# Kernel optimization log

Measured on AMD Instinct MI355X. Metric: run time of the kernel, lower is better.

Reference implementation:

```python
import jax, jax.numpy as jnp
import numpy as np

B, K, L, D = 64, 49, 200, 36  # batch, ref time points, seq len, n variables
INIT_TIME, PRIOR_HOURS = 0.0, 48.0


def setup_inputs() -> dict:
    key = jax.random.key(0)
    ks = jax.random.split(key, 9)
    X = jax.random.normal(ks[0], (B, L, D), dtype=jnp.float32)
    T = jax.random.uniform(ks[1], (B, L, D), dtype=jnp.float32) * PRIOR_HOURS
    M = (jax.random.uniform(ks[2], (B, L, D)) > 0.5).astype(jnp.float32)
    PD = jax.random.uniform(ks[3], (B, L, D), dtype=jnp.float32)
    # learned params per ALNNLayer.build (glorot-like small init)
    def glorot(k, shape):
        fan = sum(shape)
        lim = jnp.sqrt(6.0 / fan)
        return jax.random.uniform(k, shape, jnp.float32, -lim, lim)
    alpha = glorot(ks[4], (K, 1, 1))
    w_v = glorot(ks[5], (K, L, D))
    w_t = glorot(ks[6], (K, L, D, 4))
    b_v = glorot(ks[7], (K, 1, D))
    b_t = glorot(ks[8], (K, L, D, 1))
    return {"X": X, "T": T, "M": M, "PD": PD,
            "alpha": alpha, "w_v": w_v, "w_t": w_t, "b_v": b_v, "b_t": b_t}


def reference(X, T, M, PD, alpha, w_v, w_t, b_v, b_t):
    k = alpha.shape[0]
    # reference time points [K,1,1]
    ref_time = jnp.linspace(INIT_TIME, PRIOR_HOURS, k, dtype=jnp.float32).reshape(k, 1, 1)
    # broadcast [B,1,L,D] against [K,1,1] -> [B,K,L,D]
    dist = jnp.abs(T[:, None, :, :] - ref_time)           # type_distance == 'abs'
    kernel = jnp.exp(-jax.nn.relu(alpha) * dist)          # [B,K,L,D]
    intensity = jax.nn.relu(X[:, None, :, :] * kernel)    # [B,K,L,D]
    shp = intensity.shape
    # 4-channel concat on a trailing axis: [B,K,L,D,4]
    c = jnp.stack([
        jnp.broadcast_to(X[:, None, :, :], shp),
        intensity,
        jnp.broadcast_to(M[:, None, :, :], shp),
        jnp.broadcast_to(PD[:, None, :, :], shp),
    ], axis=-1)
    # stage 1: reduce_sum(w_t*c + b_t, axis=4); b_t broadcast over 4 channels -> contributes 4*b_t
    s1 = jax.nn.relu(jnp.einsum('bklds,klds->bkld', c, w_t) + 4.0 * b_t[..., 0])
    # stage 2: reduce_sum(w_v*s1 + b_v, axis=2); b_v [K,1,D] broadcast over L -> contributes L*b_v
    n_l = s1.shape[2]
    out = jax.nn.relu(jnp.einsum('bkld,kld->bkd', s1, w_v) + jnp.float32(n_l) * b_v[:, 0, :])
    return out  # [B,K,D]
```

## Files before the change

### kernel.cpp

```cpp
#include <hip/hip_runtime.h>

#define NB 64
#define NK 49
#define NL 200
#define ND 36
#define LD (NL*ND)

#define AT_FLOATS  (LD*NB*4)
#define WPK_FLOATS (LD*NK*6)
#define WPK_OFF   AT_FLOATS
#define WS_PACK_BYTES ((size_t)(AT_FLOATS + WPK_FLOATS) * 4)

#define LOG2E 1.44269504088896f

#if __has_builtin(__builtin_amdgcn_exp2f)
#define EXP2F(x) __builtin_amdgcn_exp2f(x)
#else
#define EXP2F(x) __expf((x) * 0.6931471805599453f)
#endif

__global__ __launch_bounds__(256) void alnn_pack(
    const float* __restrict__ X, const float* __restrict__ T,
    const float* __restrict__ M, const float* __restrict__ PD,
    const float* __restrict__ w_v, const float4* __restrict__ w_t,
    const float* __restrict__ b_t, float* __restrict__ ws)
{
    __shared__ float tile[9440];
    const int bid = blockIdx.x, t = threadIdx.x;

    if (bid < 225) {
        const int ld0 = bid * 32;
        const int ld = t & 31, bq = t >> 5;
        const float* src[4] = {X, T, M, PD};
        #pragma unroll
        for (int a = 0; a < 4; a++) {
            const float* A = src[a];
            for (int b = bq; b < 64; b += 8)
                tile[(a * 64 + b) * 33 + ld] = A[(size_t)b * LD + ld0 + ld];
        }
        __syncthreads();
        float4* At4 = (float4*)ws;
        const int b = t & 63, ldq = t >> 6;
        #pragma unroll
        for (int r = 0; r < 8; r++) {
            const int l_local = ldq * 8 + r;
            const int ldg = ld0 + l_local;
            const int l = ldg / ND, d = ldg - l * ND;
            float4 v;
            v.x = tile[(0 * 64 + b) * 33 + l_local];
            v.y = tile[(1 * 64 + b) * 33 + l_local];
            v.z = tile[(2 * 64 + b) * 33 + l_local];
            v.w = tile[(3 * 64 + b) * 33 + l_local];
            At4[((size_t)d * NL + l) * 64 + b] = v;
        }
    } else {
        const int ld0 = (bid - 225) * 32;
        const int ld = t & 31, kq = t >> 5;
        for (int k = kq; k < NK; k += 8) {
            const float4 wt = w_t[(size_t)k * LD + ld0 + ld];
            const float  bt = b_t[(size_t)k * LD + ld0 + ld];
            const float  wv = w_v[(size_t)k * LD + ld0 + ld];
            float* w = tile + ld * 295 + k * 6;
            w[0] = wt.x; w[1] = wt.y; w[2] = wt.z; w[3] = wt.w;
            w[4] = 4.0f * bt; w[5] = wv;
        }
        __syncthreads();
        float* Wpk = ws + WPK_OFF;
        for (int i = t; i < 7 * 32 * 42; i += 256) {
            const int ks = i / 1344, rem = i - ks * 1344;
            const int l_local = rem / 42, c = rem - l_local * 42;
            const int ldg = ld0 + l_local;
            const int l = ldg / ND, d = ldg - l * ND;
            Wpk[(((size_t)d * 7 + ks) * NL + l) * 42 + c] =
                tile[l_local * 295 + ks * 42 + c];
        }
    }
}

__global__ __launch_bounds__(1024) void alnn_main5(
    const float* __restrict__ ws_ro, const float* __restrict__ alpha,
    const float* __restrict__ b_v, float* __restrict__ out)
{
    __shared__ float red[16 * 7 * 64];

    const int orig = blockIdx.x;
    const int xcd  = orig & 7, slot = orig >> 3;
    const int base = (xcd < 4) ? xcd * 32 : 128 + (xcd - 4) * 31;
    const int job  = base + slot;

    const int d  = job / 7, ks = job - (job / 7) * 7;
    const int t  = threadIdx.x;
    const int b  = t & 63;
    const int w  = __builtin_amdgcn_readfirstlane(t >> 6);
    const int k0 = ks * 7;

    const float4* At4 = (const float4*)ws_ro + (size_t)d * NL * 64;
    const float*  Ws  = ws_ro + WPK_OFF + ((size_t)d * 7 + ks) * NL * 42;

    float arn[7], rk[7];
    #pragma unroll
    for (int kk = 0; kk < 7; kk++) {
        arn[kk] = -fmaxf(alpha[k0 + kk], 0.0f) * LOG2E;
        rk[kk]  = (float)(k0 + kk);
    }

    float acc[7] = {0, 0, 0, 0, 0, 0, 0};

    const int len  = (w < 8) ? 13 : 12;
    const int lbeg = (w < 8) ? 13 * w : 104 + 12 * (w - 8);

    for (int ll = 0; ll < len; ll++) {
        const int l = lbeg + ll;
        const float4 av = At4[(size_t)l * 64 + b];
        const float xp = fmaxf(av.x, 0.0f);
        const float* wr = Ws + (size_t)l * 42;
        #pragma unroll
        for (int kk = 0; kk < 7; kk++) {
            const float dist = fabsf(av.y - rk[kk]);
            const float e    = EXP2F(arn[kk] * dist);
            float s = fmaf(wr[kk*6+0], av.x,
                      fmaf(wr[kk*6+1], xp * e,
                      fmaf(wr[kk*6+2], av.z,
                      fmaf(wr[kk*6+3], av.w, wr[kk*6+4]))));
            acc[kk] = fmaf(wr[kk*6+5], fmaxf(s, 0.0f), acc[kk]);
        }
    }

    #pragma unroll
    for (int kk = 0; kk < 7; kk++)
        red[(w * 7 + kk) * 64 + b] = acc[kk];
    __syncthreads();

    if (w < 7) {
        const int kk = w, k = k0 + kk;
        float sum = 0.0f;
        #pragma unroll
        for (int ww = 0; ww < 16; ww++)
            sum += red[(ww * 7 + kk) * 64 + b];
        out[((size_t)b * NK + k) * ND + d] =
            fmaxf(sum + 200.0f * b_v[k * ND + d], 0.0f);
    }
}

__global__ __launch_bounds__(256) void alnn_fused_kernel(
    const float* __restrict__ X, const float* __restrict__ T,
    const float* __restrict__ M, const float* __restrict__ PD,
    const float* __restrict__ alpha, const float* __restrict__ w_v,
    const float4* __restrict__ w_t, const float* __restrict__ b_v,
    const float* __restrict__ b_t, float* __restrict__ out)
{
    const int bk = blockIdx.x;
    const int k  = bk % NK;
    const int b  = bk / NK;
    const int t  = threadIdx.x;

    __shared__ float part[7][ND];

    const float alpha_k = fmaxf(alpha[k], 0.0f);
    const float refk    = (float)k;

    if (t < 7 * ND) {
        const int d = t % ND;
        const int j = t / ND;
        const float*  Xp  = X   + (size_t)b * LD + d;
        const float*  Tp  = T   + (size_t)b * LD + d;
        const float*  Mp  = M   + (size_t)b * LD + d;
        const float*  Pp  = PD  + (size_t)b * LD + d;
        const float*  wvp = w_v + (size_t)k * LD + d;
        const float*  btp = b_t + (size_t)k * LD + d;
        const float4* wtp = w_t + (size_t)k * LD + d;

        float acc = 0.0f;
        for (int l = j; l < NL; l += 7) {
            const int o = l * ND;
            const float x  = Xp[o];
            const float tt = Tp[o];
            const float m  = Mp[o];
            const float pd = Pp[o];
            const float4 wv4 = wtp[o];
            const float bt = btp[o];
            const float dist  = fabsf(tt - refk);
            const float e     = __expf(-alpha_k * dist);
            const float inten = fmaxf(x * e, 0.0f);
            float s = fmaf(wv4.x, x, fmaf(wv4.y, inten, fmaf(wv4.z, m, fmaf(wv4.w, pd, 4.0f * bt))));
            s = fmaxf(s, 0.0f);
            acc = fmaf(wvp[o], s, acc);
        }
        part[j][d] = acc;
    }
    __syncthreads();

    if (t < ND) {
        float sum = 0.0f;
        #pragma unroll
        for (int j = 0; j < 7; ++j) sum += part[j][t];
        sum += (float)NL * b_v[k * ND + t];
        out[(size_t)bk * ND + t] = fmaxf(sum, 0.0f);
    }
}

extern "C" void kernel_launch(void* const* d_in, const int* in_sizes, int n_in,
                              void* d_out, int out_size, void* d_ws, size_t ws_size,
                              hipStream_t stream) {
    const float* X     = (const float*)d_in[0];
    const float* T     = (const float*)d_in[1];
    const float* M     = (const float*)d_in[2];
    const float* PD    = (const float*)d_in[3];
    const float* alpha = (const float*)d_in[4];
    const float* w_v   = (const float*)d_in[5];
    const float* w_t   = (const float*)d_in[6];
    const float* b_v   = (const float*)d_in[7];
    const float* b_t   = (const float*)d_in[8];
    float* out = (float*)d_out;
    float* ws  = (float*)d_ws;

    if (ws_size >= WS_PACK_BYTES) {
        alnn_pack<<<450, 256, 0, stream>>>(X, T, M, PD, w_v, (const float4*)w_t, b_t, ws);
        alnn_main5<<<252, 1024, 0, stream>>>(ws, alpha, b_v, out);
    } else {
        alnn_fused_kernel<<<NB * NK, 256, 0, stream>>>(
            X, T, M, PD, alpha, w_v, (const float4*)w_t, b_v, b_t, out);
    }
}
```

Before: 28.00 us.

## Fuse pack and main kernels into one cooperative kernel with grid sync

Replaces the two-launch pack-then-compute pipeline with a single cooperative kernel. Each block gathers its own slice of w_t/b_t/w_v directly into LDS, so the packed weight buffer in global memory is no longer written and re-read. The first 225 blocks transpose the activations into the workspace, followed by a grid-wide sync and the same compute/reduce as before. It also adds unroll-by-2 on the l loop. In exchange it adds grid-sync overhead and a large LDS footprint per block, and it depends on the cooperative launch succeeding, with a fallback to the old path if it does not.

```diff
diff --git a/kernel.cpp b/kernel.cpp
--- a/kernel.cpp
+++ b/kernel.cpp
@@ -1,4 +1,7 @@
 #include <hip/hip_runtime.h>
+#include <hip/hip_cooperative_groups.h>
+
+namespace cg = cooperative_groups;
 
 #define NB 64
 #define NK 49
@@ -9,6 +12,7 @@
 #define AT_FLOATS  (LD*NB*4)
 #define WPK_FLOATS (LD*NK*6)
 #define WPK_OFF   AT_FLOATS
+#define WS_MIN_BYTES  ((size_t)AT_FLOATS * 4)
 #define WS_PACK_BYTES ((size_t)(AT_FLOATS + WPK_FLOATS) * 4)
 
 #define LOG2E 1.44269504088896f
@@ -18,6 +22,118 @@
 #else
 #define EXP2F(x) __expf((x) * 0.6931471805599453f)
 #endif
+
+__global__ __launch_bounds__(1024, 4) void alnn_coop2(
+    const float* __restrict__ X, const float* __restrict__ T,
+    const float* __restrict__ M, const float* __restrict__ PD,
+    const float* __restrict__ alpha, const float* __restrict__ w_v,
+    const float4* __restrict__ w_t4, const float* __restrict__ b_v,
+    const float* __restrict__ b_t, float* __restrict__ out,
+    float* __restrict__ ws)
+{
+    __shared__ float tile[4 * 64 * 33];
+    __shared__ float wl[NL * 44];
+    __shared__ float red[16 * 7 * 64];
+
+    const int orig = blockIdx.x, t = threadIdx.x;
+
+    const int xcd  = orig & 7, slot = orig >> 3;
+    const int base = (xcd < 4) ? xcd * 32 : 128 + (xcd - 4) * 31;
+    const int job  = base + slot;
+    const int d = job / 7, ks = job - (job / 7) * 7;
+    const int k0 = ks * 7;
+
+    for (int i = t; i < 1400; i += 1024) {
+        const int kk = i / NL, l = i - kk * NL;
+        const size_t src = (size_t)(k0 + kk) * LD + l * ND + d;
+        const float4 wt = w_t4[src];
+        const float  bt = b_t[src];
+        const float  wv = w_v[src];
+        float* wp = wl + l * 44 + kk * 6;
+        wp[0] = wt.x; wp[1] = wt.y; wp[2] = wt.z; wp[3] = wt.w;
+        wp[4] = 4.0f * bt; wp[5] = wv;
+    }
+
+    if (orig < 225) {
+        const int ld0 = orig * 32;
+        const int ld = t & 31, bq = t >> 5;
+        const float* srcs[4] = {X, T, M, PD};
+        #pragma unroll
+        for (int a = 0; a < 4; a++) {
+            const float* A = srcs[a];
+            #pragma unroll
+            for (int b = bq; b < 64; b += 32)
+                tile[(a * 64 + b) * 33 + ld] = A[(size_t)b * LD + ld0 + ld];
+        }
+        __syncthreads();
+        float4* At4w = (float4*)ws;
+        const int b = t & 63, ldq = t >> 6;
+        #pragma unroll
+        for (int r = 0; r < 2; r++) {
+            const int ll = ldq * 2 + r;
+            const int ldg = ld0 + ll;
+            const int l = ldg / ND, dd = ldg - l * ND;
+            float4 v;
+            v.x = tile[(0 * 64 + b) * 33 + ll];
+            v.y = tile[(1 * 64 + b) * 33 + ll];
+            v.z = tile[(2 * 64 + b) * 33 + ll];
+            v.w = tile[(3 * 64 + b) * 33 + ll];
+            At4w[((size_t)dd * NL + l) * 64 + b] = v;
+        }
+    }
+
+    cg::this_grid().sync();
+
+    const int b = t & 63;
+    const int w = __builtin_amdgcn_readfirstlane(t >> 6);
+
+    const float4* At4 = (const float4*)ws + (size_t)d * NL * 64;
+
+    float arn[7], rk[7];
+    #pragma unroll
+    for (int kk = 0; kk < 7; kk++) {
+        arn[kk] = -fmaxf(alpha[k0 + kk], 0.0f) * LOG2E;
+        rk[kk]  = (float)(k0 + kk);
+    }
+
+    float acc[7] = {0, 0, 0, 0, 0, 0, 0};
+
+    const int len  = (w < 8) ? 13 : 12;
+    const int lbeg = (w < 8) ? 13 * w : 104 + 12 * (w - 8);
+
+    #pragma unroll 2
+    for (int ll = 0; ll < len; ll++) {
+        const int l = lbeg + ll;
+        const float4 av = At4[(size_t)l * 64 + b];
+        const float xp = fmaxf(av.x, 0.0f);
+        const float* wr = wl + l * 44;
+        #pragma unroll
+        for (int kk = 0; kk < 7; kk++) {
+            const float dist = fabsf(av.y - rk[kk]);
+            const float e    = EXP2F(arn[kk] * dist);
+            float s = fmaf(wr[kk*6+0], av.x,
+                      fmaf(wr[kk*6+1], xp * e,
+                      fmaf(wr[kk*6+2], av.z,
+                      fmaf(wr[kk*6+3], av.w, wr[kk*6+4]))));
+            acc[kk] = fmaf(wr[kk*6+5], fmaxf(s, 0.0f), acc[kk]);
+        }
+    }
+
+    #pragma unroll
+    for (int kk = 0; kk < 7; kk++)
+        red[(w * 7 + kk) * 64 + b] = acc[kk];
+    __syncthreads();
+
+    if (w < 7) {
+        const int kk = w, k = k0 + kk;
+        float sum = 0.0f;
+        #pragma unroll
+        for (int ww = 0; ww < 16; ww++)
+            sum += red[(ww * 7 + kk) * 64 + b];
+        out[((size_t)b * NK + k) * ND + d] =
+            fmaxf(sum + 200.0f * b_v[k * ND + d], 0.0f);
+    }
+}
 
 __global__ __launch_bounds__(256) void alnn_pack(
     const float* __restrict__ X, const float* __restrict__ T,
@@ -109,6 +225,7 @@
     const int len  = (w < 8) ? 13 : 12;
     const int lbeg = (w < 8) ? 13 * w : 104 + 12 * (w - 8);
 
+    #pragma unroll 2
     for (int ll = 0; ll < len; ll++) {
         const int l = lbeg + ll;
         const float4 av = At4[(size_t)l * 64 + b];
@@ -214,6 +331,16 @@
     float* out = (float*)d_out;
     float* ws  = (float*)d_ws;
 
+    if (ws_size >= WS_MIN_BYTES) {
+        const float4* w_t4 = (const float4*)w_t;
+        void* args[] = {(void*)&X, (void*)&T, (void*)&M, (void*)&PD, (void*)&alpha,
+                        (void*)&w_v, (void*)&w_t4, (void*)&b_v, (void*)&b_t,
+                        (void*)&out, (void*)&ws};
+        hipError_t e = hipLaunchCooperativeKernel((void*)alnn_coop2, dim3(252), dim3(1024),
+                                                  args, 0, stream);
+        if (e == hipSuccess) return;
+    }
+
     if (ws_size >= WS_PACK_BYTES) {
         alnn_pack<<<450, 256, 0, stream>>>(X, T, M, PD, w_v, (const float4*)w_t, b_t, ws);
         alnn_main5<<<252, 1024, 0, stream>>>(ws, alpha, b_v, out);
```

Measured after the change: 77.74 us. 178% more time.

## Split L dimension across two blocks with partial sums and epilogue kernel

Applied to the files above, without the earlier changes.

The main kernel's work is split in two along the sequence dimension, giving 504 blocks instead of 252 so the MI355X's compute units are better filled. Each half writes a partial sum to workspace, and a new epilogue kernel adds the two halves, the bias and the ReLU. The L loop also loads the next activation row one iteration early to hide memory latency. In exchange it adds a third kernel launch, an extra round trip of partial sums through global memory, and drops the XCD-aware job mapping.

```diff
diff --git a/kernel.cpp b/kernel.cpp
--- a/kernel.cpp
+++ b/kernel.cpp
@@ -6,10 +6,12 @@
 #define ND 36
 #define LD (NL*ND)
 
-#define AT_FLOATS  (LD*NB*4)
-#define WPK_FLOATS (LD*NK*6)
-#define WPK_OFF   AT_FLOATS
-#define WS_PACK_BYTES ((size_t)(AT_FLOATS + WPK_FLOATS) * 4)
+#define AT_FLOATS   (LD*NB*4)
+#define WPK_FLOATS  (LD*NK*6)
+#define PART_FLOATS (2*NB*NK*ND)
+#define WPK_OFF    AT_FLOATS
+#define PART_OFF   (AT_FLOATS + WPK_FLOATS)
+#define WS_NEED_BYTES ((size_t)(AT_FLOATS + WPK_FLOATS + PART_FLOATS) * 4)
 
 #define LOG2E 1.44269504088896f
 
@@ -77,18 +79,18 @@
     }
 }
 
-__global__ __launch_bounds__(1024) void alnn_main5(
+__global__ __launch_bounds__(1024, 8) void alnn_main10(
     const float* __restrict__ ws_ro, const float* __restrict__ alpha,
-    const float* __restrict__ b_v, float* __restrict__ out)
+    float* __restrict__ part)
 {
     __shared__ float red[16 * 7 * 64];
 
     const int orig = blockIdx.x;
-    const int xcd  = orig & 7, slot = orig >> 3;
-    const int base = (xcd < 4) ? xcd * 32 : 128 + (xcd - 4) * 31;
-    const int job  = base + slot;
-
-    const int d  = job / 7, ks = job - (job / 7) * 7;
+    const int job  = (orig & 7) * 63 + (orig >> 3);
+    const int d    = job / 14;
+    const int r14  = job - d * 14;
+    const int ks   = r14 >> 1, lh = r14 & 1;
+
     const int t  = threadIdx.x;
     const int b  = t & 63;
     const int w  = __builtin_amdgcn_readfirstlane(t >> 6);
@@ -106,12 +108,14 @@
 
     float acc[7] = {0, 0, 0, 0, 0, 0, 0};
 
-    const int len  = (w < 8) ? 13 : 12;
-    const int lbeg = (w < 8) ? 13 * w : 104 + 12 * (w - 8);
-
+    const int len  = (w < 4) ? 7 : 6;
+    const int lbeg = lh * 100 + ((w < 4) ? 7 * w : 28 + 6 * (w - 4));
+
+    float4 av = At4[(size_t)lbeg * 64 + b];
     for (int ll = 0; ll < len; ll++) {
         const int l = lbeg + ll;
-        const float4 av = At4[(size_t)l * 64 + b];
+        float4 nxt = av;
+        if (ll + 1 < len) nxt = At4[(size_t)(l + 1) * 64 + b];
         const float xp = fmaxf(av.x, 0.0f);
         const float* wr = Ws + (size_t)l * 42;
         #pragma unroll
@@ -124,6 +128,7 @@
                       fmaf(wr[kk*6+3], av.w, wr[kk*6+4]))));
             acc[kk] = fmaf(wr[kk*6+5], fmaxf(s, 0.0f), acc[kk]);
         }
+        av = nxt;
     }
 
     #pragma unroll
@@ -137,8 +142,19 @@
         #pragma unroll
         for (int ww = 0; ww < 16; ww++)
             sum += red[(ww * 7 + kk) * 64 + b];
-        out[((size_t)b * NK + k) * ND + d] =
-            fmaxf(sum + 200.0f * b_v[k * ND + d], 0.0f);
+        part[(size_t)lh * (NB * NK * ND) + ((size_t)b * NK + k) * ND + d] = sum;
+    }
+}
+
+__global__ __launch_bounds__(512) void alnn_epi(
+    const float* __restrict__ part, const float* __restrict__ b_v,
+    float* __restrict__ out)
+{
+    const int i = blockIdx.x * 512 + threadIdx.x;
+    if (i < NB * NK * ND) {
+        const int r = i % (NK * ND);
+        const float s = part[i] + part[NB * NK * ND + i];
+        out[i] = fmaxf(s + 200.0f * b_v[r], 0.0f);
     }
 }
 
@@ -214,9 +230,10 @@
     float* out = (float*)d_out;
     float* ws  = (float*)d_ws;
 
-    if (ws_size >= WS_PACK_BYTES) {
+    if (ws_size >= WS_NEED_BYTES) {
         alnn_pack<<<450, 256, 0, stream>>>(X, T, M, PD, w_v, (const float4*)w_t, b_t, ws);
-        alnn_main5<<<252, 1024, 0, stream>>>(ws, alpha, b_v, out);
+        alnn_main10<<<504, 1024, 0, stream>>>(ws, alpha, ws + PART_OFF);
+        alnn_epi<<<(NB * NK * ND + 511) / 512, 512, 0, stream>>>(ws + PART_OFF, b_v, out);
     } else {
         alnn_fused_kernel<<<NB * NK, 256, 0, stream>>>(
             X, T, M, PD, alpha, w_v, (const float4*)w_t, b_v, b_t, out);
```

Result: slower. 29.48 us (+5.3%).
